# Kernel optimization log

Measured on AMD Instinct MI355X. Metric: run time of the kernel, lower is better.

The kernel has to match this reference:

```python
import jax, jax.numpy as jnp
import numpy as np

N_NODES = 100000
N_EDGES = 600000
D_FEAT = 128


def setup_inputs() -> dict:
    key = jax.random.key(0)
    k1, k2, k3 = jax.random.split(key, 3)
    x = jax.random.normal(k1, (N_NODES, D_FEAT), dtype=jnp.float32)
    edge_index = jax.random.randint(k2, (2, N_EDGES), 0, N_NODES, dtype=jnp.int64)
    weight = jax.random.normal(k3, (D_FEAT, D_FEAT), dtype=jnp.float32) * (1.0 / np.sqrt(D_FEAT))
    bias = jnp.zeros((D_FEAT,), dtype=jnp.float32)
    return {"x": x, "edge_index": edge_index, "weight": weight, "bias": bias}


def gcn_conv(x, edge_index, weight, bias):
    # PyG GCNConv: h = x @ W.T; out = D^-1/2 (A + I) D^-1/2 h + b
    n = x.shape[0]
    loop = jnp.arange(n, dtype=edge_index.dtype)
    src = jnp.concatenate([edge_index[0], loop])  # message sources
    dst = jnp.concatenate([edge_index[1], loop])  # aggregation targets
    h = x @ weight.T  # [N, F]
    deg = jax.ops.segment_sum(jnp.ones_like(dst, dtype=x.dtype), dst, num_segments=n)
    dinv = jnp.where(deg > 0, jax.lax.rsqrt(deg), 0.0)
    norm = dinv[src] * dinv[dst]  # [E+N]
    agg = jax.ops.segment_sum(h[src] * norm[:, None], dst, num_segments=n)  # [N, F]
    return agg + bias


def reference(x, edge_index, weight, bias):
    return x + jax.nn.relu(gcn_conv(x, edge_index, weight, bias))
```

## Files before the change

### kernel.cpp

```cpp
#include <hip/hip_runtime.h>

#define NN  100000
#define NE  600000
#define D   128
#define CAP 32

typedef __bf16 bf16x8 __attribute__((ext_vector_type(8)));
typedef __bf16 bf16x4 __attribute__((ext_vector_type(4)));
typedef float  f32x4  __attribute__((ext_vector_type(4)));

#define GB_Z    ((NN + 1 + 255) / 256)
#define GB_WP   8
#define GB_GEMM ((NN / 16 + 3) / 4)
#define GB_FILL ((NE + 255) / 256)
#define K1_GRID (782 * 5)

__device__ inline float bflo(unsigned int v) {
    unsigned int t = v << 16; float f; __builtin_memcpy(&f, &t, 4); return f;
}
__device__ inline float bfhi(unsigned int v) {
    unsigned int t = v & 0xffff0000u; float f; __builtin_memcpy(&f, &t, 4); return f;
}

__global__ __launch_bounds__(256) void k0(int* __restrict__ cnt,
                                          const float* __restrict__ W,
                                          __bf16* __restrict__ wf,
                                          __bf16* __restrict__ g) {
    if (blockIdx.x < GB_Z) {
        int i = blockIdx.x * 256 + threadIdx.x;
        if (i <= NN) cnt[i] = 0;
    } else {
        int t = (blockIdx.x - GB_Z) * 256 + threadIdx.x;
        if (t < D) g[(size_t)NN * D + t] = (__bf16)0.f;
        int lane = t & 63, ct = (t >> 6) & 7, kt = t >> 9;
        int col = ct * 16 + (lane & 15);
        int k0  = kt * 32 + ((lane >> 4) & 3) * 8;
        const float* wp = W + col * D + k0;
        __bf16* o = wf + (size_t)t * 8;
        #pragma unroll
        for (int j = 0; j < 8; ++j) o[j] = (__bf16)wp[j];
    }
}

__global__ __launch_bounds__(256) void k1(const float* __restrict__ x,
                                          const __bf16* __restrict__ wf,
                                          const int* __restrict__ src,
                                          const int* __restrict__ dst,
                                          int* __restrict__ cnt,
                                          int* __restrict__ adj,
                                          __bf16* __restrict__ g) {
    int r  = blockIdx.x % 5;
    int gq = blockIdx.x / 5;
    if (r < 2) {
        int blk = gq * 2 + r;
        int gid = blk * 4 + (threadIdx.x >> 6);
        if (gid >= NN / 16) return;
        int lane = threadIdx.x & 63;
        int l4   = lane & 15;
        int kg   = lane >> 4;
        int node = gid * 16 + l4;

        f32x4 acc[8];
        #pragma unroll
        for (int ct = 0; ct < 8; ++ct) acc[ct] = (f32x4){0.f, 0.f, 0.f, 0.f};

        #pragma unroll
        for (int kt = 0; kt < 4; ++kt) {
            const float4* xp = (const float4*)(x + (size_t)node * D + kt * 32 + kg * 8);
            float4 x0 = xp[0];
            float4 x1 = xp[1];
            bf16x8 a;
            a[0] = (__bf16)x0.x; a[1] = (__bf16)x0.y; a[2] = (__bf16)x0.z; a[3] = (__bf16)x0.w;
            a[4] = (__bf16)x1.x; a[5] = (__bf16)x1.y; a[6] = (__bf16)x1.z; a[7] = (__bf16)x1.w;
            const bf16x8* wfp = (const bf16x8*)wf + (size_t)kt * 512 + lane;
            #pragma unroll
            for (int ct = 0; ct < 8; ++ct) {
                bf16x8 b = wfp[ct * 64];
                acc[ct] = __builtin_amdgcn_mfma_f32_16x16x32_bf16(b, a, acc[ct], 0, 0, 0);
            }
        }

        #pragma unroll
        for (int ct = 0; ct < 8; ++ct) {
            bf16x4 o;
            #pragma unroll
            for (int i = 0; i < 4; ++i) o[i] = (__bf16)acc[ct][i];
            *(bf16x4*)(g + (size_t)node * D + ct * 16 + kg * 4) = o;
        }
    } else {
        int blk = gq * 3 + (r - 2);
        int e = blk * 256 + threadIdx.x;
        if (e >= NE) return;
        int d = dst[e], s = src[e];
        if ((unsigned)d >= (unsigned)NN || (unsigned)s >= (unsigned)NN) return;
        int slot = atomicAdd(&cnt[d], 1);
        if (slot < CAP) adj[(d << 5) + slot] = s;
    }
}

__global__ __launch_bounds__(256) void k_agg(const float* __restrict__ x,
                                             const __bf16* __restrict__ g,
                                             const int* __restrict__ cnt,
                                             const float* __restrict__ bias,
                                             const int* __restrict__ adj,
                                             float* __restrict__ out) {
    int wave = blockIdx.x * 4 + (threadIdx.x >> 6);
    int lane = threadIdx.x & 63;
    int q    = lane >> 4;
    int l4   = lane & 15;
    int node = wave * 4 + q;
    int c0   = l4 * 8;

    int deg = cnt[node];
    int end = min(deg, CAP);
    float dv = rsqrtf((float)(deg + 1));
    const int* ap = adj + (node << 5);

    int4 b0 = *(const int4*)ap;
    int4 b1 = *(const int4*)(ap + 4);
    int s0 = (end > 0) ? b0.x : NN;
    int s1 = (end > 1) ? b0.y : NN;
    int s2 = (end > 2) ? b0.z : NN;
    int s3 = (end > 3) ? b0.w : NN;
    int s4 = (end > 4) ? b1.x : NN;
    int s5 = (end > 5) ? b1.y : NN;
    int s6 = (end > 6) ? b1.z : NN;
    int s7 = (end > 7) ? b1.w : NN;

    const float4* xp = (const float4*)(x + (size_t)node * D + c0);
    float4 xv0 = xp[0], xv1 = xp[1];
    const float4* bp = (const float4*)(bias + c0);
    float4 bv0 = bp[0], bv1 = bp[1];

    uint4 u = *(const uint4*)(g + (size_t)node * D + c0);
    int n0 = cnt[s0], n1 = cnt[s1], n2 = cnt[s2], n3 = cnt[s3];
    int n4 = cnt[s4], n5 = cnt[s5], n6 = cnt[s6], n7 = cnt[s7];
    uint4 v0 = *(const uint4*)(g + (size_t)s0 * D + c0);
    uint4 v1 = *(const uint4*)(g + (size_t)s1 * D + c0);
    uint4 v2 = *(const uint4*)(g + (size_t)s2 * D + c0);
    uint4 v3 = *(const uint4*)(g + (size_t)s3 * D + c0);
    uint4 v4 = *(const uint4*)(g + (size_t)s4 * D + c0);
    uint4 v5 = *(const uint4*)(g + (size_t)s5 * D + c0);
    uint4 v6 = *(const uint4*)(g + (size_t)s6 * D + c0);
    uint4 v7 = *(const uint4*)(g + (size_t)s7 * D + c0);

    float a0 = dv * bflo(u.x), a1 = dv * bfhi(u.x), a2 = dv * bflo(u.y), a3 = dv * bfhi(u.y);
    float a4 = dv * bflo(u.z), a5 = dv * bfhi(u.z), a6 = dv * bflo(u.w), a7 = dv * bfhi(u.w);

    float w0 = rsqrtf((float)(n0 + 1)), w1 = rsqrtf((float)(n1 + 1));
    float w2 = rsqrtf((float)(n2 + 1)), w3 = rsqrtf((float)(n3 + 1));
    float w4 = rsqrtf((float)(n4 + 1)), w5 = rsqrtf((float)(n5 + 1));
    float w6 = rsqrtf((float)(n6 + 1)), w7 = rsqrtf((float)(n7 + 1));

    a0 += w0 * bflo(v0.x); a1 += w0 * bfhi(v0.x); a2 += w0 * bflo(v0.y); a3 += w0 * bfhi(v0.y);
    a4 += w0 * bflo(v0.z); a5 += w0 * bfhi(v0.z); a6 += w0 * bflo(v0.w); a7 += w0 * bfhi(v0.w);
    a0 += w1 * bflo(v1.x); a1 += w1 * bfhi(v1.x); a2 += w1 * bflo(v1.y); a3 += w1 * bfhi(v1.y);
    a4 += w1 * bflo(v1.z); a5 += w1 * bfhi(v1.z); a6 += w1 * bflo(v1.w); a7 += w1 * bfhi(v1.w);
    a0 += w2 * bflo(v2.x); a1 += w2 * bfhi(v2.x); a2 += w2 * bflo(v2.y); a3 += w2 * bfhi(v2.y);
    a4 += w2 * bflo(v2.z); a5 += w2 * bfhi(v2.z); a6 += w2 * bflo(v2.w); a7 += w2 * bfhi(v2.w);
    a0 += w3 * bflo(v3.x); a1 += w3 * bfhi(v3.x); a2 += w3 * bflo(v3.y); a3 += w3 * bfhi(v3.y);
    a4 += w3 * bflo(v3.z); a5 += w3 * bfhi(v3.z); a6 += w3 * bflo(v3.w); a7 += w3 * bfhi(v3.w);
    a0 += w4 * bflo(v4.x); a1 += w4 * bfhi(v4.x); a2 += w4 * bflo(v4.y); a3 += w4 * bfhi(v4.y);
    a4 += w4 * bflo(v4.z); a5 += w4 * bfhi(v4.z); a6 += w4 * bflo(v4.w); a7 += w4 * bfhi(v4.w);
    a0 += w5 * bflo(v5.x); a1 += w5 * bfhi(v5.x); a2 += w5 * bflo(v5.y); a3 += w5 * bfhi(v5.y);
    a4 += w5 * bflo(v5.z); a5 += w5 * bfhi(v5.z); a6 += w5 * bflo(v5.w); a7 += w5 * bfhi(v5.w);
    a0 += w6 * bflo(v6.x); a1 += w6 * bfhi(v6.x); a2 += w6 * bflo(v6.y); a3 += w6 * bfhi(v6.y);
    a4 += w6 * bflo(v6.z); a5 += w6 * bfhi(v6.z); a6 += w6 * bflo(v6.w); a7 += w6 * bfhi(v6.w);
    a0 += w7 * bflo(v7.x); a1 += w7 * bfhi(v7.x); a2 += w7 * bflo(v7.y); a3 += w7 * bfhi(v7.y);
    a4 += w7 * bflo(v7.z); a5 += w7 * bfhi(v7.z); a6 += w7 * bflo(v7.w); a7 += w7 * bfhi(v7.w);

    for (int i = 8; i < end; i += 4) {
        int t0 = ap[i];
        int t1 = (i + 1 < end) ? ap[i + 1] : NN;
        int t2 = (i + 2 < end) ? ap[i + 2] : NN;
        int t3 = (i + 3 < end) ? ap[i + 3] : NN;
        int m0 = cnt[t0], m1 = cnt[t1], m2 = cnt[t2], m3 = cnt[t3];
        uint4 y0 = *(const uint4*)(g + (size_t)t0 * D + c0);
        uint4 y1 = *(const uint4*)(g + (size_t)t1 * D + c0);
        uint4 y2 = *(const uint4*)(g + (size_t)t2 * D + c0);
        uint4 y3 = *(const uint4*)(g + (size_t)t3 * D + c0);
        float z0 = rsqrtf((float)(m0 + 1));
        float z1 = rsqrtf((float)(m1 + 1));
        float z2 = rsqrtf((float)(m2 + 1));
        float z3 = rsqrtf((float)(m3 + 1));
        a0 += z0 * bflo(y0.x); a1 += z0 * bfhi(y0.x); a2 += z0 * bflo(y0.y); a3 += z0 * bfhi(y0.y);
        a4 += z0 * bflo(y0.z); a5 += z0 * bfhi(y0.z); a6 += z0 * bflo(y0.w); a7 += z0 * bfhi(y0.w);
        a0 += z1 * bflo(y1.x); a1 += z1 * bfhi(y1.x); a2 += z1 * bflo(y1.y); a3 += z1 * bfhi(y1.y);
        a4 += z1 * bflo(y1.z); a5 += z1 * bfhi(y1.z); a6 += z1 * bflo(y1.w); a7 += z1 * bfhi(y1.w);
        a0 += z2 * bflo(y2.x); a1 += z2 * bfhi(y2.x); a2 += z2 * bflo(y2.y); a3 += z2 * bfhi(y2.y);
        a4 += z2 * bflo(y2.z); a5 += z2 * bfhi(y2.z); a6 += z2 * bflo(y2.w); a7 += z2 * bfhi(y2.w);
        a0 += z3 * bflo(y3.x); a1 += z3 * bfhi(y3.x); a2 += z3 * bflo(y3.y); a3 += z3 * bfhi(y3.y);
        a4 += z3 * bflo(y3.z); a5 += z3 * bfhi(y3.z); a6 += z3 * bflo(y3.w); a7 += z3 * bfhi(y3.w);
    }

    f32x4 r0, r1;
    r0[0] = xv0.x + fmaxf(fmaf(dv, a0, bv0.x), 0.f);
    r0[1] = xv0.y + fmaxf(fmaf(dv, a1, bv0.y), 0.f);
    r0[2] = xv0.z + fmaxf(fmaf(dv, a2, bv0.z), 0.f);
    r0[3] = xv0.w + fmaxf(fmaf(dv, a3, bv0.w), 0.f);
    r1[0] = xv1.x + fmaxf(fmaf(dv, a4, bv1.x), 0.f);
    r1[1] = xv1.y + fmaxf(fmaf(dv, a5, bv1.y), 0.f);
    r1[2] = xv1.z + fmaxf(fmaf(dv, a6, bv1.z), 0.f);
    r1[3] = xv1.w + fmaxf(fmaf(dv, a7, bv1.w), 0.f);
    f32x4* op = (f32x4*)(out + (size_t)node * D + c0);
    __builtin_nontemporal_store(r0, op);
    __builtin_nontemporal_store(r1, op + 1);
}

extern "C" void kernel_launch(void* const* d_in, const int* in_sizes, int n_in,
                              void* d_out, int out_size, void* d_ws, size_t ws_size,
                              hipStream_t stream) {
    const float* x    = (const float*)d_in[0];
    const int*   ei   = (const int*)d_in[1];
    const float* W    = (const float*)d_in[2];
    const float* bias = (const float*)d_in[3];
    float* out = (float*)d_out;

    const int* src = ei;
    const int* dst = ei + NE;

    char* p = (char*)d_ws;
    auto take = [&](size_t bytes) {
        char* q = p;
        p += (bytes + 255) & ~(size_t)255;
        return q;
    };
    int*    cnt = (int*)take((size_t)(NN + 1) * 4);
    int*    adj = (int*)take((size_t)NN * CAP * 4);
    __bf16* wf  = (__bf16*)take((size_t)2048 * 8 * 2);
    __bf16* g   = (__bf16*)take((size_t)(NN + 1) * D * 2);

    k0   <<<GB_Z + GB_WP, 256, 0, stream>>>(cnt, W, wf, g);
    k1   <<<K1_GRID, 256, 0, stream>>>(x, wf, src, dst, cnt, adj, g);
    k_agg<<<NN / 16, 256, 0, stream>>>(x, g, cnt, bias, adj, out);
}
```

Measured before the change: 84.42 us.

## Prefill adjacency with sentinel, stage GEMM output via LDS, decouple agg gathers from degree

The adjacency table is now pre-filled with the sentinel node index in k0, so the aggregation kernel can issue neighbor gathers straight from the adjacency loads without first waiting on the degree load and masking. The GEMM epilogue stages bf16 results through shared memory so each lane writes full 16-byte contiguous row segments, and x is read with nontemporal loads. The trade-off is an extra 12.8 MB memset of the adjacency array in k0 and extra LDS traffic in the GEMM.

```diff
diff --git a/kernel.cpp b/kernel.cpp
--- a/kernel.cpp
+++ b/kernel.cpp
@@ -9,11 +9,10 @@
 typedef __bf16 bf16x4 __attribute__((ext_vector_type(4)));
 typedef float  f32x4  __attribute__((ext_vector_type(4)));
 
-#define GB_Z    ((NN + 1 + 255) / 256)
-#define GB_WP   8
-#define GB_GEMM ((NN / 16 + 3) / 4)
-#define GB_FILL ((NE + 255) / 256)
-#define K1_GRID (782 * 5)
+#define GB_Z      ((NN + 1 + 255) / 256)
+#define GB_AI     ((NN * CAP / 4) / 256)
+#define GB_WP     8
+#define K1_GRID   (782 * 5)
 
 __device__ inline float bflo(unsigned int v) {
     unsigned int t = v << 16; float f; __builtin_memcpy(&f, &t, 4); return f;
@@ -23,14 +22,18 @@
 }
 
 __global__ __launch_bounds__(256) void k0(int* __restrict__ cnt,
+                                          int4* __restrict__ adj4,
                                           const float* __restrict__ W,
                                           __bf16* __restrict__ wf,
                                           __bf16* __restrict__ g) {
     if (blockIdx.x < GB_Z) {
         int i = blockIdx.x * 256 + threadIdx.x;
         if (i <= NN) cnt[i] = 0;
+    } else if (blockIdx.x < GB_Z + GB_AI) {
+        int i = (blockIdx.x - GB_Z) * 256 + threadIdx.x;
+        adj4[i] = make_int4(NN, NN, NN, NN);
     } else {
-        int t = (blockIdx.x - GB_Z) * 256 + threadIdx.x;
+        int t = (blockIdx.x - GB_Z - GB_AI) * 256 + threadIdx.x;
         if (t < D) g[(size_t)NN * D + t] = (__bf16)0.f;
         int lane = t & 63, ct = (t >> 6) & 7, kt = t >> 9;
         int col = ct * 16 + (lane & 15);
@@ -49,16 +52,19 @@
                                           int* __restrict__ cnt,
                                           int* __restrict__ adj,
                                           __bf16* __restrict__ g) {
+    __shared__ __align__(16) unsigned stg[4][16][68];
     int r  = blockIdx.x % 5;
     int gq = blockIdx.x / 5;
     if (r < 2) {
         int blk = gq * 2 + r;
         int gid = blk * 4 + (threadIdx.x >> 6);
         if (gid >= NN / 16) return;
+        int w    = threadIdx.x >> 6;
         int lane = threadIdx.x & 63;
         int l4   = lane & 15;
         int kg   = lane >> 4;
-        int node = gid * 16 + l4;
+        int row0 = gid * 16;
+        int node = row0 + l4;
 
         f32x4 acc[8];
         #pragma unroll
@@ -66,12 +72,12 @@
 
         #pragma unroll
         for (int kt = 0; kt < 4; ++kt) {
-            const float4* xp = (const float4*)(x + (size_t)node * D + kt * 32 + kg * 8);
-            float4 x0 = xp[0];
-            float4 x1 = xp[1];
+            const f32x4* xp = (const f32x4*)(x + (size_t)node * D + kt * 32 + kg * 8);
+            f32x4 x0 = __builtin_nontemporal_load(xp);
+            f32x4 x1 = __builtin_nontemporal_load(xp + 1);
             bf16x8 a;
-            a[0] = (__bf16)x0.x; a[1] = (__bf16)x0.y; a[2] = (__bf16)x0.z; a[3] = (__bf16)x0.w;
-            a[4] = (__bf16)x1.x; a[5] = (__bf16)x1.y; a[6] = (__bf16)x1.z; a[7] = (__bf16)x1.w;
+            a[0] = (__bf16)x0[0]; a[1] = (__bf16)x0[1]; a[2] = (__bf16)x0[2]; a[3] = (__bf16)x0[3];
+            a[4] = (__bf16)x1[0]; a[5] = (__bf16)x1[1]; a[6] = (__bf16)x1[2]; a[7] = (__bf16)x1[3];
             const bf16x8* wfp = (const bf16x8*)wf + (size_t)kt * 512 + lane;
             #pragma unroll
             for (int ct = 0; ct < 8; ++ct) {
@@ -82,10 +88,17 @@
 
         #pragma unroll
         for (int ct = 0; ct < 8; ++ct) {
-            bf16x4 o;
+            union { bf16x4 v; uint2 u; } o;
             #pragma unroll
-            for (int i = 0; i < 4; ++i) o[i] = (__bf16)acc[ct][i];
-            *(bf16x4*)(g + (size_t)node * D + ct * 16 + kg * 4) = o;
+            for (int i = 0; i < 4; ++i) o.v[i] = (__bf16)acc[ct][i];
+            stg[w][l4][ct * 8 + kg * 2]     = o.u.x;
+            stg[w][l4][ct * 8 + kg * 2 + 1] = o.u.y;
+        }
+        #pragma unroll
+        for (int j = 0; j < 4; ++j) {
+            int rr = j * 4 + kg;
+            uint4 dvec = *(const uint4*)&stg[w][rr][l4 * 4];
+            *(uint4*)(g + (size_t)(row0 + rr) * D + l4 * 8) = dvec;
         }
     } else {
         int blk = gq * 3 + (r - 2);
@@ -111,28 +124,14 @@
     int node = wave * 4 + q;
     int c0   = l4 * 8;
 
-    int deg = cnt[node];
-    int end = min(deg, CAP);
-    float dv = rsqrtf((float)(deg + 1));
     const int* ap = adj + (node << 5);
-
     int4 b0 = *(const int4*)ap;
     int4 b1 = *(const int4*)(ap + 4);
-    int s0 = (end > 0) ? b0.x : NN;
-    int s1 = (end > 1) ? b0.y : NN;
-    int s2 = (end > 2) ? b0.z : NN;
-    int s3 = (end > 3) ? b0.w : NN;
-    int s4 = (end > 4) ? b1.x : NN;
-    int s5 = (end > 5) ? b1.y : NN;
-    int s6 = (end > 6) ? b1.z : NN;
-    int s7 = (end > 7) ? b1.w : NN;
-
-    const float4* xp = (const float4*)(x + (size_t)node * D + c0);
-    float4 xv0 = xp[0], xv1 = xp[1];
-    const float4* bp = (const float4*)(bias + c0);
-    float4 bv0 = bp[0], bv1 = bp[1];
-
-    uint4 u = *(const uint4*)(g + (size_t)node * D + c0);
+    int deg = cnt[node];
+
+    int s0 = b0.x, s1 = b0.y, s2 = b0.z, s3 = b0.w;
+    int s4 = b1.x, s5 = b1.y, s6 = b1.z, s7 = b1.w;
+
     int n0 = cnt[s0], n1 = cnt[s1], n2 = cnt[s2], n3 = cnt[s3];
     int n4 = cnt[s4], n5 = cnt[s5], n6 = cnt[s6], n7 = cnt[s7];
     uint4 v0 = *(const uint4*)(g + (size_t)s0 * D + c0);
@@ -143,7 +142,14 @@
     uint4 v5 = *(const uint4*)(g + (size_t)s5 * D + c0);
     uint4 v6 = *(const uint4*)(g + (size_t)s6 * D + c0);
     uint4 v7 = *(const uint4*)(g + (size_t)s7 * D + c0);
-
+    uint4 u  = *(const uint4*)(g + (size_t)node * D + c0);
+
+    const float4* xp = (const float4*)(x + (size_t)node * D + c0);
+    float4 xv0 = xp[0], xv1 = xp[1];
+    const float4* bp = (const float4*)(bias + c0);
+    float4 bv0 = bp[0], bv1 = bp[1];
+
+    float dv = rsqrtf((float)(deg + 1));
     float a0 = dv * bflo(u.x), a1 = dv * bfhi(u.x), a2 = dv * bflo(u.y), a3 = dv * bfhi(u.y);
     float a4 = dv * bflo(u.z), a5 = dv * bfhi(u.z), a6 = dv * bflo(u.w), a7 = dv * bfhi(u.w);
 
@@ -169,11 +175,9 @@
     a0 += w7 * bflo(v7.x); a1 += w7 * bfhi(v7.x); a2 += w7 * bflo(v7.y); a3 += w7 * bfhi(v7.y);
     a4 += w7 * bflo(v7.z); a5 += w7 * bfhi(v7.z); a6 += w7 * bflo(v7.w); a7 += w7 * bfhi(v7.w);
 
+    int end = min(deg, CAP);
     for (int i = 8; i < end; i += 4) {
-        int t0 = ap[i];
-        int t1 = (i + 1 < end) ? ap[i + 1] : NN;
-        int t2 = (i + 2 < end) ? ap[i + 2] : NN;
-        int t3 = (i + 3 < end) ? ap[i + 3] : NN;
+        int t0 = ap[i], t1 = ap[i + 1], t2 = ap[i + 2], t3 = ap[i + 3];
         int m0 = cnt[t0], m1 = cnt[t1], m2 = cnt[t2], m3 = cnt[t3];
         uint4 y0 = *(const uint4*)(g + (size_t)t0 * D + c0);
         uint4 y1 = *(const uint4*)(g + (size_t)t1 * D + c0);
@@ -230,7 +234,7 @@
     __bf16* wf  = (__bf16*)take((size_t)2048 * 8 * 2);
     __bf16* g   = (__bf16*)take((size_t)(NN + 1) * D * 2);
 
-    k0   <<<GB_Z + GB_WP, 256, 0, stream>>>(cnt, W, wf, g);
+    k0   <<<GB_Z + GB_AI + GB_WP, 256, 0, stream>>>(cnt, (int4*)adj, W, wf, g);
     k1   <<<K1_GRID, 256, 0, stream>>>(x, wf, src, dst, cnt, adj, g);
     k_agg<<<NN / 16, 256, 0, stream>>>(x, g, cnt, bias, adj, out);
 }
```

After: 93.38 us. +10.6%, slower.
